# Optimization experiments

Hardware: AMD Instinct MI355X
Metric: run time of the kernel (lower is better)

Reference implementation:

```python
import jax, jax.numpy as jnp
import numpy as np

EMBED_DIM = 512
NUM_HEADS = 8
HEAD_DIM = EMBED_DIM // NUM_HEADS
GRID_SHAPE = (48, 48)
WINDOW = (16, 16)
BATCH = 2
SEQ = GRID_SHAPE[0] * GRID_SHAPE[1]
NEG = float(np.finfo(np.float16).min)  # matches torch.finfo(torch.float16).min fill


def build_window_mask():
    # replicates: indices = np.indices(grid).flatten(1).T; dist = |i-j|*2; all(dist < window)
    idx = np.indices(GRID_SHAPE).reshape(len(GRID_SHAPE), -1).T  # [N, 2]
    dist = np.abs(idx[:, None, :] - idx[None, :, :]) * 2          # [N, N, 2]
    mask = np.all(dist < np.array(WINDOW)[None, None, :], axis=-1)  # [N, N] bool
    return jnp.asarray(mask)


def setup_inputs() -> dict:
    key = jax.random.key(0)
    ks = jax.random.split(key, 11)
    s = 1.0 / np.sqrt(EMBED_DIM)
    inp = {
        "x_q": jax.random.normal(ks[0], (BATCH, SEQ, EMBED_DIM), jnp.float32),
        "x_k": jax.random.normal(ks[1], (BATCH, SEQ, EMBED_DIM), jnp.float32),
        "x_v": jax.random.normal(ks[2], (BATCH, SEQ, EMBED_DIM), jnp.float32),
        "Wq": jax.random.normal(ks[3], (EMBED_DIM, EMBED_DIM), jnp.float32) * s,
        "bq": jnp.zeros((EMBED_DIM,), jnp.float32),
        "Wk": jax.random.normal(ks[4], (EMBED_DIM, EMBED_DIM), jnp.float32) * s,
        "bk": jnp.zeros((EMBED_DIM,), jnp.float32),
        "Wv": jax.random.normal(ks[5], (EMBED_DIM, EMBED_DIM), jnp.float32) * s,
        "bv": jnp.zeros((EMBED_DIM,), jnp.float32),
        "Wo": jax.random.normal(ks[6], (EMBED_DIM, EMBED_DIM), jnp.float32) * s,
        "bo": jnp.zeros((EMBED_DIM,), jnp.float32),
        "attn_mask": build_window_mask(),
    }
    return inp


def reference(x_q, x_k, x_v, Wq, bq, Wk, bk, Wv, bv, Wo, bo, attn_mask):
    B, S, E = x_q.shape
    H, D = NUM_HEADS, HEAD_DIM

    def proj(x, W, b):
        y = x @ W.T + b                         # [B,S,E]
        return y.reshape(B, S, H, D).transpose(0, 2, 1, 3)  # [B,H,S,D]

    q = proj(x_q, Wq, bq)
    k = proj(x_k, Wk, bk)
    v = proj(x_v, Wv, bv)

    scores = jnp.einsum("bhqd,bhkd->bhqk", q, k) / np.sqrt(D)
    # Windowed branch: per-row gather over allowed keys + softmax == dense
    # softmax with disallowed keys masked to a huge negative value.
    scores = jnp.where(attn_mask[None, None, :, :], scores, NEG)
    probs = jax.nn.softmax(scores, axis=-1)     # dropout=0.0 -> identity
    context = jnp.einsum("bhqk,bhkd->bhqd", probs, v)
    context = context.transpose(0, 2, 1, 3).reshape(B, S, E)
    out = context @ Wo.T + bo
    return out
```

## Files before the change

kernel.cpp:

```cpp
#include <hip/hip_runtime.h>

typedef __attribute__((ext_vector_type(8))) short short8;
typedef __attribute__((ext_vector_type(4))) float f32x4;
typedef __attribute__((ext_vector_type(2))) unsigned int u32x2;
typedef __attribute__((ext_vector_type(4))) unsigned int u32x4;

#define DEV __device__ __forceinline__

#define QH_E 0L
#define KH_E 2359296L
#define VT_E 4718592L
#define CTX_E 7077888L

#define LOG2E 1.4426950408889634f

#define BARRIER() __builtin_amdgcn_s_barrier()
#define SCHED0() __builtin_amdgcn_sched_barrier(0)

DEV unsigned short f2bf(float f) {
  unsigned int x = __float_as_uint(f);
  x = (x + 0x7fffu + ((x >> 16) & 1u)) >> 16;
  return (unsigned short)x;
}

DEV unsigned int pk2(float a, float b) {
  unsigned int r;
  asm("v_cvt_pk_bf16_f32 %0, %1, %2" : "=v"(r) : "v"(a), "v"(b));
  return r;
}

DEV void gl2lds16(const unsigned short* g, unsigned short* l) {
  __builtin_amdgcn_global_load_lds(
      (const __attribute__((address_space(1))) unsigned int*)g,
      (__attribute__((address_space(3))) unsigned int*)l, 16, 0, 0);
}

DEV f32x4 mfma16(short8 a, short8 b, f32x4 c) {
  return __builtin_amdgcn_mfma_f32_16x16x32_bf16(a, b, c, 0, 0, 0);
}

template <int MI, int AF32>
DEV void gemm_rs(const float* __restrict__ Af, const unsigned short* __restrict__ Ab,
                 const float* __restrict__ W, int m0, int n0,
                 unsigned short* ldsA, unsigned short* ldsB, f32x4 acc[][2]) {
  const int tid = threadIdx.x;
  const int lane = tid & 63, wvv = tid >> 6;
  const int g = lane >> 4, qi = lane & 15;
  const int wr = wvv >> 1, wc = wvv & 1;
  const int c8 = tid & 7;
  const int rbase = tid >> 3;
  const int j8 = ((c8 ^ (rbase & 7))) * 8;
  f32x4 ra[MI][2];
  u32x4 rab[MI];
  f32x4 rw[2][2];
#pragma unroll
  for (int mi = 0; mi < MI; ++mi)
#pragma unroll
    for (int ni = 0; ni < 2; ++ni) {
      f32x4 z = {0.f, 0.f, 0.f, 0.f};
      acc[mi][ni] = z;
    }
#define RS_LOADS(kt) do {                                                     \
    const int k0_ = (kt) * 64;                                                \
    if (AF32) {                                                               \
      _Pragma("unroll")                                                       \
      for (int it = 0; it < MI; ++it) {                                       \
        const float* p = Af + (long)(m0 + it * 32 + rbase) * 512 + k0_ + j8;  \
        ra[it][0] = *(const f32x4*)p;                                         \
        ra[it][1] = *(const f32x4*)(p + 4);                                   \
      }                                                                       \
    } else {                                                                  \
      _Pragma("unroll")                                                       \
      for (int it = 0; it < MI; ++it)                                         \
        rab[it] = *(const u32x4*)(Ab + (long)(m0 + it * 32 + rbase) * 512 +   \
                                  k0_ + j8);                                  \
    }                                                                         \
    _Pragma("unroll")                                                         \
    for (int it = 0; it < 2; ++it) {                                          \
      const float* p = W + (long)(n0 + it * 32 + rbase) * 512 + k0_ + j8;     \
      rw[it][0] = *(const f32x4*)p;                                           \
      rw[it][1] = *(const f32x4*)(p + 4);                                     \
    }                                                                         \
  } while (0)
#define RS_WRITES(bi) do {                                                    \
    _Pragma("unroll")                                                         \
    for (int it = 0; it < MI; ++it) {                                         \
      u32x4 v_;                                                               \
      if (AF32) {                                                             \
        v_.x = pk2(ra[it][0].x, ra[it][0].y);                                 \
        v_.y = pk2(ra[it][0].z, ra[it][0].w);                                 \
        v_.z = pk2(ra[it][1].x, ra[it][1].y);                                 \
        v_.w = pk2(ra[it][1].z, ra[it][1].w);                                 \
      } else v_ = rab[it];                                                    \
      *(u32x4*)(ldsA + (bi) * (MI * 2048) + (it * 256 + tid) * 8) = v_;       \
    }                                                                         \
    _Pragma("unroll")                                                         \
    for (int it = 0; it < 2; ++it) {                                          \
      u32x4 v_;                                                               \
      v_.x = pk2(rw[it][0].x, rw[it][0].y);                                   \
      v_.y = pk2(rw[it][0].z, rw[it][0].w);                                   \
      v_.z = pk2(rw[it][1].x, rw[it][1].y);                                   \
      v_.w = pk2(rw[it][1].z, rw[it][1].w);                                   \
      *(u32x4*)(ldsB + (bi) * 4096 + (it * 256 + tid) * 8) = v_;              \
    }                                                                         \
  } while (0)
  RS_LOADS(0);
  RS_WRITES(0);
  RS_LOADS(1);
  asm volatile("s_waitcnt lgkmcnt(0)" ::: "memory");
  BARRIER();
  SCHED0();
#pragma unroll
  for (int kt = 0; kt < 8; ++kt) {
    const unsigned short* La = ldsA + (kt & 1) * (MI * 2048);
    const unsigned short* Lb = ldsB + (kt & 1) * 4096;
    __builtin_amdgcn_s_setprio(1);
#pragma unroll
    for (int kk = 0; kk < 2; ++kk) {
      short8 af[MI], bfr[2];
#pragma unroll
      for (int mi = 0; mi < MI; ++mi) {
        int row = MI * 16 * wr + 16 * mi + qi;
        int c16 = (4 * kk + g) ^ (qi & 7);
        af[mi] = *(const short8*)(La + row * 64 + c16 * 8);
      }
#pragma unroll
      for (int ni = 0; ni < 2; ++ni) {
        int row = 32 * wc + 16 * ni + qi;
        int c16 = (4 * kk + g) ^ (qi & 7);
        bfr[ni] = *(const short8*)(Lb + row * 64 + c16 * 8);
      }
#pragma unroll
      for (int mi = 0; mi < MI; ++mi)
#pragma unroll
        for (int ni = 0; ni < 2; ++ni)
          acc[mi][ni] = mfma16(af[mi], bfr[ni], acc[mi][ni]);
    }
    __builtin_amdgcn_s_setprio(0);
    SCHED0();
    if (kt < 7) RS_WRITES((kt + 1) & 1);
    if (kt < 6) RS_LOADS(kt + 2);
    if (kt < 7) {
      asm volatile("s_waitcnt lgkmcnt(0)" ::: "memory");
      BARRIER();
      SCHED0();
    }
  }
#undef RS_LOADS
#undef RS_WRITES
}

__global__ __launch_bounds__(256, 3) void proj_qkv_kernel(
    const float* __restrict__ xq, const float* __restrict__ xk,
    const float* __restrict__ xv, const float* __restrict__ wqp,
    const float* __restrict__ wkp, const float* __restrict__ wvp,
    const float* __restrict__ bq, const float* __restrict__ bk,
    const float* __restrict__ bv, unsigned short* __restrict__ ws) {
  __shared__ unsigned short ldsA[2 * 8192];
  __shared__ unsigned short ldsB[2 * 4096];
  int f = blockIdx.x;
  int wid = (f & 7) * 108 + (f >> 3);
  const int z = wid / 288;
  const int rem = wid % 288;
  const int m0 = (rem >> 3) * 128, n0 = (rem & 7) * 64;
  const float *A, *W, *bias;
  unsigned short* dst;
  float oscale;
  int mode;
  if (z == 0)      { A = xq; W = wqp; bias = bq; oscale = 0.125f * LOG2E; dst = ws + QH_E; mode = 0; }
  else if (z == 1) { A = xk; W = wkp; bias = bk; oscale = 1.0f;           dst = ws + KH_E; mode = 0; }
  else             { A = xv; W = wvp; bias = bv; oscale = 1.0f;           dst = ws + VT_E; mode = 1; }
  f32x4 acc[4][2];
  gemm_rs<4, 1>(A, nullptr, W, m0, n0, ldsA, ldsB, acc);
  const int lane = threadIdx.x & 63, wvv = threadIdx.x >> 6;
  const int g = lane >> 4, qi = lane & 15;
  const int wr = wvv >> 1, wc = wvv & 1;
#pragma unroll
  for (int ni = 0; ni < 2; ++ni) {
    int n = n0 + 32 * wc + 16 * ni + qi;
    float bb = bias[n];
    int h = n >> 6, d = n & 63;
#pragma unroll
    for (int mi = 0; mi < 4; ++mi) {
      int m = m0 + 64 * wr + 16 * mi + 4 * g;
      int b = (m >= 2304) ? 1 : 0;
      int s = m - b * 2304;
      if (mode == 0) {
#pragma unroll
        for (int r = 0; r < 4; ++r) {
          float v = (acc[mi][ni][r] + bb) * oscale;
          dst[((long)((b * 8 + h) * 2304 + s + r)) * 64 + d] = f2bf(v);
        }
      } else {
        u32x2 o;
        o.x = pk2(acc[mi][ni][0] + bb, acc[mi][ni][1] + bb);
        o.y = pk2(acc[mi][ni][2] + bb, acc[mi][ni][3] + bb);
        *(u32x2*)(dst + ((long)((b * 8 + h) * 64 + d)) * 2304 + s) = o;
      }
    }
  }
}

__global__ __launch_bounds__(256, 3) void proj_out_kernel(
    const unsigned short* __restrict__ ws, const float* __restrict__ wop,
    const float* __restrict__ bo, float* __restrict__ out) {
  __shared__ unsigned short ldsA[2 * 4096];
  __shared__ unsigned short ldsB[2 * 4096];
  int f = blockIdx.x;
  int wid = (f & 7) * 72 + (f >> 3);
  const int m0 = (wid >> 3) * 64, n0 = (wid & 7) * 64;
  f32x4 acc[2][2];
  gemm_rs<2, 0>(nullptr, ws + CTX_E, wop, m0, n0, ldsA, ldsB, acc);
  const int lane = threadIdx.x & 63, wvv = threadIdx.x >> 6;
  const int g = lane >> 4, qi = lane & 15;
  const int wr = wvv >> 1, wc = wvv & 1;
#pragma unroll
  for (int ni = 0; ni < 2; ++ni) {
    int n = n0 + 32 * wc + 16 * ni + qi;
    float bb = bo[n];
#pragma unroll
    for (int mi = 0; mi < 2; ++mi) {
#pragma unroll
      for (int r = 0; r < 4; ++r) {
        int m = m0 + 32 * wr + 16 * mi + 4 * g + r;
        out[(long)m * 512 + n] = acc[mi][ni][r] + bb;
      }
    }
  }
}

__global__ __launch_bounds__(192) void attn_kernel(unsigned short* __restrict__ ws) {
  __shared__ unsigned short ldsKV[3 * 7168];
  __shared__ unsigned short ldsP[3][16][72];
  __shared__ unsigned short ldsDum[512];
  const int tid = threadIdx.x;
  const int lane = tid & 63, wv = tid >> 6;
  const int g = lane >> 4, qi = lane & 15;
  int f = blockIdx.x;
  int wid = (f & 7) * 96 + (f >> 3);
  const int bh = wid / 48, r = wid - 48 * bh;
  const int ci = wv * 16 + qi;
  const unsigned short* Kh = ws + KH_E + (long)bh * 2304 * 64;
  const unsigned short* Vt = ws + VT_E + (long)bh * 64 * 2304;
  const int q = r * 48 + ci;
  const unsigned short* qp = ws + QH_E + ((long)bh * 2304 + q) * 64;
  f32x4 qraw0 = *(const f32x4*)(qp + 8 * g);
  f32x4 qraw1 = *(const f32x4*)(qp + 32 + 8 * g);
  asm volatile("" : "+v"(qraw0), "+v"(qraw1));
  short8 qf0 = __builtin_bit_cast(short8, qraw0);
  short8 qf1 = __builtin_bit_cast(short8, qraw1);
  float msk[12];
#pragma unroll
  for (int mb = 0; mb < 3; ++mb)
#pragma unroll
    for (int rr = 0; rr < 4; ++rr) {
      int cj = 16 * mb + 4 * g + rr;
      msk[mb * 4 + rr] = ((unsigned)(ci - cj + 7) <= 14u) ? 0.f : -1e30f;
    }
  {
    u32x2 z2; z2.x = 0u; z2.y = 0u;
    *(u32x2*)(&ldsP[wv][qi][48 + 4 * g]) = z2;
  }
  f32x4 cacc[4];
#pragma unroll
  for (int mb = 0; mb < 4; ++mb) { f32x4 z = {0.f, 0.f, 0.f, 0.f}; cacc[mb] = z; }
  float lrun = 0.f;

#define ASTAGE(bi, rj) do {                                                   \
    unsigned short* Lb_ = ldsKV + (bi) * 7168;                                \
    const unsigned short* Ks_ = Kh + (long)(rj) * 3072;                       \
    _Pragma("unroll")                                                         \
    for (int it = 0; it < 5; ++it) {                                          \
      int u = it * 192 + tid;                                                 \
      if (u < 384) {                                                          \
        int kr = u >> 3, c = u & 7, cs = c ^ (kr & 7);                        \
        gl2lds16(Ks_ + kr * 64 + cs * 8, Lb_ + u * 8);                        \
      } else if (u < 896) {                                                   \
        int v2 = u - 384;                                                     \
        int d = v2 >> 3, c = v2 & 7, cs = c ^ (d & 7);                        \
        long jb = (long)(rj) * 48 + cs * 8;                                   \
        if (jb > 2296) jb = 2296;                                             \
        gl2lds16(Vt + (long)d * 2304 + jb, Lb_ + u * 8);                      \
      } else {                                                                \
        gl2lds16(Kh + (u - 896) * 8, ldsDum + (u - 896) * 8);                 \
      }                                                                       \
    }                                                                         \
  } while (0)

  const int rlo = (r > 7) ? r - 7 : 0;
  const int rhi = (r < 40) ? r + 7 : 47;
  const int nch = rhi - rlo + 1;
  ASTAGE(0, rlo);
  ASTAGE(1, rlo + 1);
  for (int t = 0; t < nch; ++t) {
    if (t + 2 < nch) ASTAGE((t + 2) % 3, rlo + t + 2);
    if (t + 3 <= nch)      { asm volatile("s_waitcnt vmcnt(10)" ::: "memory"); }
    else if (t + 2 == nch) { asm volatile("s_waitcnt vmcnt(5)" ::: "memory"); }
    else                   { asm volatile("s_waitcnt vmcnt(0)" ::: "memory"); }
    BARRIER();
    SCHED0();
    const unsigned short* Kt = ldsKV + (t % 3) * 7168;
    const unsigned short* Vm = Kt + 3072;
    f32x4 sacc[3];
#pragma unroll
    for (int mb = 0; mb < 3; ++mb) { f32x4 z = {0.f, 0.f, 0.f, 0.f}; sacc[mb] = z; }
    __builtin_amdgcn_s_setprio(1);
#pragma unroll
    for (int kk = 0; kk < 2; ++kk) {
      short8 qf = kk ? qf1 : qf0;
#pragma unroll
      for (int mb = 0; mb < 3; ++mb) {
        int row = 16 * mb + qi;
        int c16 = (4 * kk + g) ^ (qi & 7);
        short8 ka = *(const short8*)(Kt + row * 64 + c16 * 8);
        sacc[mb] = mfma16(ka, qf, sacc[mb]);
      }
    }
    __builtin_amdgcn_s_setprio(0);
    unsigned int pw[6];
#pragma unroll
    for (int mb = 0; mb < 3; ++mb) {
      float p0 = __builtin_amdgcn_exp2f(sacc[mb][0] + msk[mb * 4 + 0]);
      float p1 = __builtin_amdgcn_exp2f(sacc[mb][1] + msk[mb * 4 + 1]);
      float p2 = __builtin_amdgcn_exp2f(sacc[mb][2] + msk[mb * 4 + 2]);
      float p3 = __builtin_amdgcn_exp2f(sacc[mb][3] + msk[mb * 4 + 3]);
      lrun += (p0 + p1) + (p2 + p3);
      pw[2 * mb] = pk2(p0, p1);
      pw[2 * mb + 1] = pk2(p2, p3);
    }
#pragma unroll
    for (int mb = 0; mb < 3; ++mb) {
      u32x2 pv2; pv2.x = pw[2 * mb]; pv2.y = pw[2 * mb + 1];
      *(u32x2*)(&ldsP[wv][qi][16 * mb + 4 * g]) = pv2;
    }
    __builtin_amdgcn_s_setprio(1);
#pragma unroll
    for (int kk = 0; kk < 2; ++kk) {
      short8 pb = *(const short8*)(&ldsP[wv][qi][32 * kk + 8 * g]);
#pragma unroll
      for (int mb = 0; mb < 4; ++mb) {
        int row = 16 * mb + qi;
        int c16 = (4 * kk + g) ^ (qi & 7);
        short8 va = *(const short8*)(Vm + row * 64 + c16 * 8);
        cacc[mb] = mfma16(va, pb, cacc[mb]);
      }
    }
    __builtin_amdgcn_s_setprio(0);
    BARRIER();
    SCHED0();
  }
#undef ASTAGE
  lrun += __shfl_xor(lrun, 16);
  lrun += __shfl_xor(lrun, 32);
  const float inv = 1.0f / lrun;
  unsigned short* ctx = ws + CTX_E;
  const int b2 = bh >> 3, h2 = bh & 7;
#pragma unroll
  for (int mb = 0; mb < 4; ++mb) {
    u32x2 o;
    o.x = pk2(cacc[mb][0] * inv, cacc[mb][1] * inv);
    o.y = pk2(cacc[mb][2] * inv, cacc[mb][3] * inv);
    long off = ((long)(b2 * 2304 + q)) * 512 + h2 * 64 + 16 * mb + 4 * g;
    *(u32x2*)(ctx + off) = o;
  }
}

extern "C" void kernel_launch(void* const* d_in, const int* in_sizes, int n_in,
                              void* d_out, int out_size, void* d_ws, size_t ws_size,
                              hipStream_t stream) {
  const float* xq = (const float*)d_in[0];
  const float* xk = (const float*)d_in[1];
  const float* xv = (const float*)d_in[2];
  const float* wq = (const float*)d_in[3];
  const float* bq = (const float*)d_in[4];
  const float* wk = (const float*)d_in[5];
  const float* bk = (const float*)d_in[6];
  const float* wv = (const float*)d_in[7];
  const float* bv = (const float*)d_in[8];
  const float* wo = (const float*)d_in[9];
  const float* bo = (const float*)d_in[10];
  unsigned short* ws = (unsigned short*)d_ws;
  float* out = (float*)d_out;

  proj_qkv_kernel<<<dim3(864), dim3(256), 0, stream>>>(xq, xk, xv, wq, wk, wv,
                                                       bq, bk, bv, ws);
  attn_kernel<<<dim3(768), dim3(192), 0, stream>>>(ws);
  proj_out_kernel<<<dim3(576), dim3(256), 0, stream>>>(ws, wo, bo, out);
}
```

Baseline: 57.50 us.

## Deepen prefetch pipelines in projection GEMMs and drop trailing attention barrier

The QKV projection now prefetches weight tiles one extra k-step ahead with double-buffered registers. The output projection moves to a triple-buffered LDS ring with loads issued four steps ahead. The attention loop now issues the next-stage async copy after the top barrier, which lets it remove the end-of-iteration barrier. These changes aim to hide global-load latency and cut a barrier per chunk, at the cost of more registers and LDS that may reduce occupancy.

```diff
diff --git a/kernel.cpp b/kernel.cpp
--- a/kernel.cpp
+++ b/kernel.cpp
@@ -39,88 +39,81 @@
   return __builtin_amdgcn_mfma_f32_16x16x32_bf16(a, b, c, 0, 0, 0);
 }
 
-template <int MI, int AF32>
-DEV void gemm_rs(const float* __restrict__ Af, const unsigned short* __restrict__ Ab,
-                 const float* __restrict__ W, int m0, int n0,
-                 unsigned short* ldsA, unsigned short* ldsB, f32x4 acc[][2]) {
+DEV void gemm_qkv(const float* __restrict__ A, const float* __restrict__ W,
+                  int m0, int n0, unsigned short* ldsA, unsigned short* ldsB,
+                  f32x4 acc[4][2]) {
   const int tid = threadIdx.x;
   const int lane = tid & 63, wvv = tid >> 6;
   const int g = lane >> 4, qi = lane & 15;
   const int wr = wvv >> 1, wc = wvv & 1;
-  const int c8 = tid & 7;
-  const int rbase = tid >> 3;
-  const int j8 = ((c8 ^ (rbase & 7))) * 8;
-  f32x4 ra[MI][2];
-  u32x4 rab[MI];
-  f32x4 rw[2][2];
-#pragma unroll
-  for (int mi = 0; mi < MI; ++mi)
+  const int c8 = tid & 7, rbase = tid >> 3;
+  const int j8 = (c8 ^ (rbase & 7)) * 8;
+  f32x4 ra[4][2];
+  f32x4 rw[2][2][2];
+#pragma unroll
+  for (int mi = 0; mi < 4; ++mi)
 #pragma unroll
     for (int ni = 0; ni < 2; ++ni) {
       f32x4 z = {0.f, 0.f, 0.f, 0.f};
       acc[mi][ni] = z;
     }
-#define RS_LOADS(kt) do {                                                     \
+#define QLA(kt) do {                                                          \
     const int k0_ = (kt) * 64;                                                \
-    if (AF32) {                                                               \
-      _Pragma("unroll")                                                       \
-      for (int it = 0; it < MI; ++it) {                                       \
-        const float* p = Af + (long)(m0 + it * 32 + rbase) * 512 + k0_ + j8;  \
-        ra[it][0] = *(const f32x4*)p;                                         \
-        ra[it][1] = *(const f32x4*)(p + 4);                                   \
-      }                                                                       \
-    } else {                                                                  \
-      _Pragma("unroll")                                                       \
-      for (int it = 0; it < MI; ++it)                                         \
-        rab[it] = *(const u32x4*)(Ab + (long)(m0 + it * 32 + rbase) * 512 +   \
-                                  k0_ + j8);                                  \
-    }                                                                         \
+    _Pragma("unroll")                                                         \
+    for (int it = 0; it < 4; ++it) {                                          \
+      const float* p = A + (long)(m0 + it * 32 + rbase) * 512 + k0_ + j8;     \
+      ra[it][0] = *(const f32x4*)p;                                           \
+      ra[it][1] = *(const f32x4*)(p + 4);                                     \
+    }                                                                         \
+  } while (0)
+#define QLB(kt) do {                                                          \
+    const int k0_ = (kt) * 64;                                                \
     _Pragma("unroll")                                                         \
     for (int it = 0; it < 2; ++it) {                                          \
       const float* p = W + (long)(n0 + it * 32 + rbase) * 512 + k0_ + j8;     \
-      rw[it][0] = *(const f32x4*)p;                                           \
-      rw[it][1] = *(const f32x4*)(p + 4);                                     \
-    }                                                                         \
-  } while (0)
-#define RS_WRITES(bi) do {                                                    \
-    _Pragma("unroll")                                                         \
-    for (int it = 0; it < MI; ++it) {                                         \
+      rw[(kt) & 1][it][0] = *(const f32x4*)p;                                 \
+      rw[(kt) & 1][it][1] = *(const f32x4*)(p + 4);                           \
+    }                                                                         \
+  } while (0)
+#define QWA(bi) do {                                                          \
+    _Pragma("unroll")                                                         \
+    for (int it = 0; it < 4; ++it) {                                          \
       u32x4 v_;                                                               \
-      if (AF32) {                                                             \
-        v_.x = pk2(ra[it][0].x, ra[it][0].y);                                 \
-        v_.y = pk2(ra[it][0].z, ra[it][0].w);                                 \
-        v_.z = pk2(ra[it][1].x, ra[it][1].y);                                 \
-        v_.w = pk2(ra[it][1].z, ra[it][1].w);                                 \
-      } else v_ = rab[it];                                                    \
-      *(u32x4*)(ldsA + (bi) * (MI * 2048) + (it * 256 + tid) * 8) = v_;       \
-    }                                                                         \
+      v_.x = pk2(ra[it][0].x, ra[it][0].y);                                   \
+      v_.y = pk2(ra[it][0].z, ra[it][0].w);                                   \
+      v_.z = pk2(ra[it][1].x, ra[it][1].y);                                   \
+      v_.w = pk2(ra[it][1].z, ra[it][1].w);                                   \
+      *(u32x4*)(ldsA + (bi) * 8192 + (it * 256 + tid) * 8) = v_;              \
+    }                                                                         \
+  } while (0)
+#define QWB(bi) do {                                                          \
     _Pragma("unroll")                                                         \
     for (int it = 0; it < 2; ++it) {                                          \
       u32x4 v_;                                                               \
-      v_.x = pk2(rw[it][0].x, rw[it][0].y);                                   \
-      v_.y = pk2(rw[it][0].z, rw[it][0].w);                                   \
-      v_.z = pk2(rw[it][1].x, rw[it][1].y);                                   \
-      v_.w = pk2(rw[it][1].z, rw[it][1].w);                                   \
+      v_.x = pk2(rw[(bi)][it][0].x, rw[(bi)][it][0].y);                       \
+      v_.y = pk2(rw[(bi)][it][0].z, rw[(bi)][it][0].w);                       \
+      v_.z = pk2(rw[(bi)][it][1].x, rw[(bi)][it][1].y);                       \
+      v_.w = pk2(rw[(bi)][it][1].z, rw[(bi)][it][1].w);                       \
       *(u32x4*)(ldsB + (bi) * 4096 + (it * 256 + tid) * 8) = v_;              \
     }                                                                         \
   } while (0)
-  RS_LOADS(0);
-  RS_WRITES(0);
-  RS_LOADS(1);
+  QLA(0); QLB(0); QLB(1);
+  QWA(0); QWB(0);
+  QLA(1); QLB(2);
   asm volatile("s_waitcnt lgkmcnt(0)" ::: "memory");
   BARRIER();
   SCHED0();
 #pragma unroll
   for (int kt = 0; kt < 8; ++kt) {
-    const unsigned short* La = ldsA + (kt & 1) * (MI * 2048);
+    const unsigned short* La = ldsA + (kt & 1) * 8192;
     const unsigned short* Lb = ldsB + (kt & 1) * 4096;
     __builtin_amdgcn_s_setprio(1);
 #pragma unroll
     for (int kk = 0; kk < 2; ++kk) {
-      short8 af[MI], bfr[2];
-#pragma unroll
-      for (int mi = 0; mi < MI; ++mi) {
-        int row = MI * 16 * wr + 16 * mi + qi;
+      short8 af[4], bfr[2];
+#pragma unroll
+      for (int mi = 0; mi < 4; ++mi) {
+        int row = 64 * wr + 16 * mi + qi;
         int c16 = (4 * kk + g) ^ (qi & 7);
         af[mi] = *(const short8*)(La + row * 64 + c16 * 8);
       }
@@ -131,23 +124,125 @@
         bfr[ni] = *(const short8*)(Lb + row * 64 + c16 * 8);
       }
 #pragma unroll
-      for (int mi = 0; mi < MI; ++mi)
+      for (int mi = 0; mi < 4; ++mi)
 #pragma unroll
         for (int ni = 0; ni < 2; ++ni)
           acc[mi][ni] = mfma16(af[mi], bfr[ni], acc[mi][ni]);
     }
     __builtin_amdgcn_s_setprio(0);
     SCHED0();
-    if (kt < 7) RS_WRITES((kt + 1) & 1);
-    if (kt < 6) RS_LOADS(kt + 2);
+    if (kt < 7) { QWA((kt + 1) & 1); QWB((kt + 1) & 1); }
+    if (kt < 6) QLA(kt + 2);
+    if (kt < 5) QLB(kt + 3);
     if (kt < 7) {
       asm volatile("s_waitcnt lgkmcnt(0)" ::: "memory");
       BARRIER();
       SCHED0();
     }
   }
-#undef RS_LOADS
-#undef RS_WRITES
+#undef QLA
+#undef QLB
+#undef QWA
+#undef QWB
+}
+
+DEV void gemm_o(const unsigned short* __restrict__ A, const float* __restrict__ W,
+                int m0, int n0, unsigned short* ldsA, unsigned short* ldsB,
+                f32x4 acc[2][2]) {
+  const int tid = threadIdx.x;
+  const int lane = tid & 63, wvv = tid >> 6;
+  const int g = lane >> 4, qi = lane & 15;
+  const int wr = wvv >> 1, wc = wvv & 1;
+  const int c8 = tid & 7, rbase = tid >> 3;
+  const int j8 = (c8 ^ (rbase & 7)) * 8;
+  u32x4 rab[2][2];
+  f32x4 rw[2][2][2];
+#pragma unroll
+  for (int mi = 0; mi < 2; ++mi)
+#pragma unroll
+    for (int ni = 0; ni < 2; ++ni) {
+      f32x4 z = {0.f, 0.f, 0.f, 0.f};
+      acc[mi][ni] = z;
+    }
+#define OLA(kt) do {                                                          \
+    const int k0_ = (kt) * 64;                                                \
+    _Pragma("unroll")                                                         \
+    for (int it = 0; it < 2; ++it)                                            \
+      rab[(kt) & 1][it] =                                                     \
+          *(const u32x4*)(A + (long)(m0 + it * 32 + rbase) * 512 + k0_ + j8); \
+  } while (0)
+#define OLB(kt) do {                                                          \
+    const int k0_ = (kt) * 64;                                                \
+    _Pragma("unroll")                                                         \
+    for (int it = 0; it < 2; ++it) {                                          \
+      const float* p = W + (long)(n0 + it * 32 + rbase) * 512 + k0_ + j8;     \
+      rw[(kt) & 1][it][0] = *(const f32x4*)p;                                 \
+      rw[(kt) & 1][it][1] = *(const f32x4*)(p + 4);                           \
+    }                                                                         \
+  } while (0)
+#define OW(kt) do {                                                           \
+    const int b3_ = (kt) % 3, s_ = (kt) & 1;                                  \
+    _Pragma("unroll")                                                         \
+    for (int it = 0; it < 2; ++it)                                            \
+      *(u32x4*)(ldsA + b3_ * 4096 + (it * 256 + tid) * 8) = rab[s_][it];      \
+    _Pragma("unroll")                                                         \
+    for (int it = 0; it < 2; ++it) {                                          \
+      u32x4 v_;                                                               \
+      v_.x = pk2(rw[s_][it][0].x, rw[s_][it][0].y);                           \
+      v_.y = pk2(rw[s_][it][0].z, rw[s_][it][0].w);                           \
+      v_.z = pk2(rw[s_][it][1].x, rw[s_][it][1].y);                           \
+      v_.w = pk2(rw[s_][it][1].z, rw[s_][it][1].w);                           \
+      *(u32x4*)(ldsB + b3_ * 4096 + (it * 256 + tid) * 8) = v_;               \
+    }                                                                         \
+  } while (0)
+  OLA(0); OLB(0);
+  OLA(1); OLB(1);
+  OW(0);
+  OLA(2); OLB(2);
+  OW(1);
+  OLA(3); OLB(3);
+  asm volatile("s_waitcnt lgkmcnt(0)" ::: "memory");
+  BARRIER();
+  SCHED0();
+#pragma unroll
+  for (int kt = 0; kt < 8; ++kt) {
+    const unsigned short* La = ldsA + (kt % 3) * 4096;
+    const unsigned short* Lb = ldsB + (kt % 3) * 4096;
+    __builtin_amdgcn_s_setprio(1);
+#pragma unroll
+    for (int kk = 0; kk < 2; ++kk) {
+      short8 af[2], bfr[2];
+#pragma unroll
+      for (int mi = 0; mi < 2; ++mi) {
+        int row = 32 * wr + 16 * mi + qi;
+        int c16 = (4 * kk + g) ^ (qi & 7);
+        af[mi] = *(const short8*)(La + row * 64 + c16 * 8);
+      }
+#pragma unroll
+      for (int ni = 0; ni < 2; ++ni) {
+        int row = 32 * wc + 16 * ni + qi;
+        int c16 = (4 * kk + g) ^ (qi & 7);
+        bfr[ni] = *(const short8*)(Lb + row * 64 + c16 * 8);
+      }
+#pragma unroll
+      for (int mi = 0; mi < 2; ++mi)
+#pragma unroll
+        for (int ni = 0; ni < 2; ++ni)
+          acc[mi][ni] = mfma16(af[mi], bfr[ni], acc[mi][ni]);
+    }
+    __builtin_amdgcn_s_setprio(0);
+    SCHED0();
+    if (kt < 6) OW(kt + 2);
+    if (kt < 4) { OLA(kt + 4); OLB(kt + 4); }
+    if (kt < 7) {
+      asm volatile("s_waitcnt lgkmcnt(0)" ::: "memory");
+      BARRIER();
+      SCHED0();
+    }
+  }
+#undef OLA
+#undef OLB
+#undef OW
 }
 
 __global__ __launch_bounds__(256, 3) void proj_qkv_kernel(
@@ -171,7 +266,7 @@
   else if (z == 1) { A = xk; W = wkp; bias = bk; oscale = 1.0f;           dst = ws + KH_E; mode = 0; }
   else             { A = xv; W = wvp; bias = bv; oscale = 1.0f;           dst = ws + VT_E; mode = 1; }
   f32x4 acc[4][2];
-  gemm_rs<4, 1>(A, nullptr, W, m0, n0, ldsA, ldsB, acc);
+  gemm_qkv(A, W, m0, n0, ldsA, ldsB, acc);
   const int lane = threadIdx.x & 63, wvv = threadIdx.x >> 6;
   const int g = lane >> 4, qi = lane & 15;
   const int wr = wvv >> 1, wc = wvv & 1;
@@ -204,13 +299,13 @@
 __global__ __launch_bounds__(256, 3) void proj_out_kernel(
     const unsigned short* __restrict__ ws, const float* __restrict__ wop,
     const float* __restrict__ bo, float* __restrict__ out) {
-  __shared__ unsigned short ldsA[2 * 4096];
-  __shared__ unsigned short ldsB[2 * 4096];
+  __shared__ unsigned short ldsA[3 * 4096];
+  __shared__ unsigned short ldsB[3 * 4096];
   int f = blockIdx.x;
   int wid = (f & 7) * 72 + (f >> 3);
   const int m0 = (wid >> 3) * 64, n0 = (wid & 7) * 64;
   f32x4 acc[2][2];
-  gemm_rs<2, 0>(nullptr, ws + CTX_E, wop, m0, n0, ldsA, ldsB, acc);
+  gemm_o(ws + CTX_E, wop, m0, n0, ldsA, ldsB, acc);
   const int lane = threadIdx.x & 63, wvv = threadIdx.x >> 6;
   const int g = lane >> 4, qi = lane & 15;
   const int wr = wvv >> 1, wc = wvv & 1;
@@ -293,12 +388,11 @@
   ASTAGE(0, rlo);
   ASTAGE(1, rlo + 1);
   for (int t = 0; t < nch; ++t) {
-    if (t + 2 < nch) ASTAGE((t + 2) % 3, rlo + t + 2);
-    if (t + 3 <= nch)      { asm volatile("s_waitcnt vmcnt(10)" ::: "memory"); }
-    else if (t + 2 == nch) { asm volatile("s_waitcnt vmcnt(5)" ::: "memory"); }
-    else                   { asm volatile("s_waitcnt vmcnt(0)" ::: "memory"); }
+    if (t + 1 < nch) { asm volatile("s_waitcnt vmcnt(5)" ::: "memory"); }
+    else             { asm volatile("s_waitcnt vmcnt(0)" ::: "memory"); }
     BARRIER();
     SCHED0();
+    if (t + 2 < nch) ASTAGE((t + 2) % 3, rlo + t + 2);
     const unsigned short* Kt = ldsKV + (t % 3) * 7168;
     const unsigned short* Vm = Kt + 3072;
     f32x4 sacc[3];
@@ -346,8 +440,6 @@
       }
     }
     __builtin_amdgcn_s_setprio(0);
-    BARRIER();
-    SCHED0();
   }
 #undef ASTAGE
   lrun += __shfl_xor(lrun, 16);
```

After: 57.49 us. No clear change (-0.0%).
